# Kernel optimization log

Hardware: AMD Instinct MI355X
Metric: run time of the kernel (lower is better)

The kernel has to match this reference:

```python
import jax, jax.numpy as jnp
import numpy as np

HEADS = 64
VOCAB = 5
EPS = 1e-5

def _layer_norm(x, g, b):
    mu = jnp.mean(x, axis=-1, keepdims=True)
    var = jnp.var(x, axis=-1, keepdims=True)
    return (x - mu) * jax.lax.rsqrt(var + EPS) * g + b

def setup_inputs() -> dict:
    key = jax.random.key(0)
    ks = jax.random.split(key, 12)
    h = HEADS
    s = 1.0 / np.sqrt(h)
    return {
        "x": jax.random.normal(ks[0], (8, 384, 384, h), dtype=jnp.float32),
        "W1": jax.random.normal(ks[1], (h, h), dtype=jnp.float32) * s,
        "b1": jnp.zeros((h,), jnp.float32),
        "W2": jax.random.normal(ks[2], (h, h), dtype=jnp.float32) * s,
        "b2": jnp.zeros((h,), jnp.float32),
        "W3": jax.random.normal(ks[3], (h, h), dtype=jnp.float32) * s,
        "b3": jnp.zeros((h,), jnp.float32),
        "ln_g": jnp.ones((h,), jnp.float32),
        "ln_b": jnp.zeros((h,), jnp.float32),
        "Wo": jax.random.normal(ks[4], (h, VOCAB), dtype=jnp.float32) * s,
        "bo": jnp.zeros((VOCAB,), jnp.float32),
    }

def reference(x, W1, b1, W2, b2, W3, b3, ln_g, ln_b, Wo, bo):
    # three (Linear -> gelu -> shared LayerNorm) blocks on [b,s,s,h]
    h = _layer_norm(jax.nn.gelu(x @ W1 + b1, approximate=False), ln_g, ln_b)
    h = _layer_norm(jax.nn.gelu(h @ W2 + b2, approximate=False), ln_g, ln_b)
    h = _layer_norm(jax.nn.gelu(h @ W3 + b3, approximate=False), ln_g, ln_b)
    out = h @ Wo + bo  # [b,s,s,vocab]
    return (out + jnp.swapaxes(out, 1, 2)) * 0.5
```

## Files before the change

kernel.cpp:

```cpp
#include <hip/hip_runtime.h>
#include <cstdint>
#include <cstddef>

typedef __attribute__((ext_vector_type(8))) __bf16   bf16x8;
typedef __attribute__((ext_vector_type(2))) __bf16   bf16x2;
typedef __attribute__((ext_vector_type(4))) float    f32x4;
typedef __attribute__((ext_vector_type(4))) uint32_t u32x4;

#define N_ROWS   1179648
#define N_TILES  73728
#define BLOCKS   2048
#define TPW      9
#define SDIM     384
#define VOCAB    5

#define WO_OFF   24576
#define BIAS_OFF 26624
#define OUT_OFF  27392

__device__ __forceinline__ f32x4 gelu4(f32x4 x){
  f32x4 u = x * x;
  f32x4 w = u * (-0.10294456f) + (-2.3021255f);
  f32x4 z = x * w;
  f32x4 e;
  e[0] = __builtin_amdgcn_exp2f(z[0]);
  e[1] = __builtin_amdgcn_exp2f(z[1]);
  e[2] = __builtin_amdgcn_exp2f(z[2]);
  e[3] = __builtin_amdgcn_exp2f(z[3]);
  f32x4 d = e + 1.0f;
  f32x4 r;
  r[0] = __builtin_amdgcn_rcpf(d[0]);
  r[1] = __builtin_amdgcn_rcpf(d[1]);
  r[2] = __builtin_amdgcn_rcpf(d[2]);
  r[3] = __builtin_amdgcn_rcpf(d[3]);
  return x * r;
}

__device__ __forceinline__ bf16x8 mk_bf8(f32x4 a, f32x4 b){
  bf16x8 v;
  v[0]=(__bf16)a[0]; v[1]=(__bf16)a[1]; v[2]=(__bf16)a[2]; v[3]=(__bf16)a[3];
  v[4]=(__bf16)b[0]; v[5]=(__bf16)b[1]; v[6]=(__bf16)b[2]; v[7]=(__bf16)b[3];
  return v;
}

__device__ __forceinline__ int perm_rho(int m){
  return (m & 0x23) | ((m & 4) << 2) | ((m & 0x18) >> 1);
}

__global__ __launch_bounds__(256)
void mlp_kernel(const float* __restrict__ x,
                const float* __restrict__ W1, const float* __restrict__ b1,
                const float* __restrict__ W2, const float* __restrict__ b2,
                const float* __restrict__ W3, const float* __restrict__ b3,
                const float* __restrict__ lng, const float* __restrict__ lnb,
                const float* __restrict__ Wo,  const float* __restrict__ bo,
                float* __restrict__ tmp)
{
  __shared__ __align__(16) uint8_t Wl[28672];

  const int tid = threadIdx.x;

  {
    int m = tid & 63, g = tid >> 6;
    int rho = perm_rho(m);
    uint8_t* wrow = Wl + rho * 128;
    int swz = (rho & 7) << 4;
    #pragma unroll 1
    for (int idx = g; idx < 96; idx += 4) {
      int L = idx >> 5, kp = idx & 31;
      const float* W = (L == 0) ? W1 : ((L == 1) ? W2 : W3);
      float lo = W[(2 * kp    ) * 64 + m];
      float hi = W[(2 * kp + 1) * 64 + m];
      bf16x2 p = { (__bf16)lo, (__bf16)hi };
      *(uint32_t*)(wrow + L * 8192 + ((4 * kp) ^ swz)) = __builtin_bit_cast(uint32_t, p);
    }
    int mm = tid & 15;
    #pragma unroll 1
    for (int kp = tid >> 4; kp < 32; kp += 16) {
      float lo = (mm < VOCAB) ? Wo[(2 * kp    ) * VOCAB + mm] : 0.0f;
      float hi = (mm < VOCAB) ? Wo[(2 * kp + 1) * VOCAB + mm] : 0.0f;
      bf16x2 p = { (__bf16)lo, (__bf16)hi };
      *(uint32_t*)(Wl + WO_OFF + mm * 128 + ((4 * kp) ^ ((mm & 7) << 4))) =
          __builtin_bit_cast(uint32_t, p);
    }
    if (tid < 192) {
      float v = (tid < 64) ? b1[tid] : ((tid < 128) ? b2[tid - 64] : b3[tid - 128]);
      *(float*)(Wl + BIAS_OFF + tid * 4) = v;
    }
  }
  __syncthreads();

  const int wav  = tid >> 6, lane = tid & 63;
  const int h    = lane >> 4;
  const int b    = lane & 15;
  const int swzW = (b & 7) << 4;
  const int rowB = b * 128;
  const int kOff = 16 * h;
  const float* biasL = (const float*)(Wl + BIAS_OFF);
  float* myF = (float*)(Wl + OUT_OFF) + wav * 80;

  f32x4 ggr[4], bbr[4], aoInit;
  #pragma unroll
  for (int mt = 0; mt < 4; ++mt) {
    int base = 8 * h + 4 * (mt & 1) + 32 * (mt >> 1);
    ggr[mt] = *(const f32x4*)(lng + base);
    bbr[mt] = *(const f32x4*)(lnb + base);
  }
  #pragma unroll
  for (int r = 0; r < 4; ++r) {
    int v = 4 * h + r;
    aoInit[r] = (v < VOCAB) ? bo[v] : 0.0f;
  }

  const int gw = blockIdx.x * 4 + wav;
  int t = gw * TPW;

  f32x4 xn[4];
  {
    const float* px = x + (size_t)(t * 16 + b) * 64 + 8 * h;
    xn[0] = *(const f32x4*)(px);      xn[1] = *(const f32x4*)(px + 4);
    xn[2] = *(const f32x4*)(px + 32); xn[3] = *(const f32x4*)(px + 36);
  }

  #pragma unroll 1
  for (int i = 0; i < TPW; ++i, ++t) {
    u32x4 bfr[2];
    bfr[0] = __builtin_bit_cast(u32x4, mk_bf8(xn[0], xn[1]));
    bfr[1] = __builtin_bit_cast(u32x4, mk_bf8(xn[2], xn[3]));

    {
      int tn = (i + 1 < TPW) ? (t + 1) : t;
      const float* pn = x + (size_t)(tn * 16 + b) * 64 + 8 * h;
      xn[0] = *(const f32x4*)(pn);      xn[1] = *(const f32x4*)(pn + 4);
      xn[2] = *(const f32x4*)(pn + 32); xn[3] = *(const f32x4*)(pn + 36);
    }

    #pragma unroll
    for (int L = 0; L < 3; ++L) {
      const uint8_t* wp = Wl + L * 8192 + rowB;
      f32x4 acc[4];
      #pragma unroll
      for (int mt = 0; mt < 4; ++mt) {
        u32x4 w0 = *(const u32x4*)(wp + mt * 2048 + ((kOff     ) ^ swzW));
        u32x4 w1 = *(const u32x4*)(wp + mt * 2048 + ((kOff + 64) ^ swzW));
        int base = 8 * h + 4 * (mt & 1) + 32 * (mt >> 1);
        acc[mt] = *(const f32x4*)(biasL + L * 64 + base);
        acc[mt] = __builtin_amdgcn_mfma_f32_16x16x32_bf16(
            __builtin_bit_cast(bf16x8, w0), __builtin_bit_cast(bf16x8, bfr[0]), acc[mt], 0, 0, 0);
        acc[mt] = __builtin_amdgcn_mfma_f32_16x16x32_bf16(
            __builtin_bit_cast(bf16x8, w1), __builtin_bit_cast(bf16x8, bfr[1]), acc[mt], 0, 0, 0);
      }

      #pragma unroll
      for (int mt = 0; mt < 4; ++mt) acc[mt] = gelu4(acc[mt]);

      f32x4 vs = acc[0] + acc[1] + acc[2] + acc[3];
      f32x4 vq = acc[0]*acc[0] + acc[1]*acc[1] + acc[2]*acc[2] + acc[3]*acc[3];
      float s1 = (vs[0]+vs[1]) + (vs[2]+vs[3]);
      float s2 = (vq[0]+vq[1]) + (vq[2]+vq[3]);
      s1 += __shfl_xor(s1, 16); s2 += __shfl_xor(s2, 16);
      s1 += __shfl_xor(s1, 32); s2 += __shfl_xor(s2, 32);
      float mu   = s1 * (1.0f/64.0f);
      float var  = __builtin_fmaf(s2, (1.0f/64.0f), -mu * mu);
      float rstd = rsqrtf(var + 1e-5f);
      float nm   = -mu * rstd;

      f32x4 n0 = (acc[0] * rstd + nm) * ggr[0] + bbr[0];
      f32x4 n1 = (acc[1] * rstd + nm) * ggr[1] + bbr[1];
      f32x4 n2 = (acc[2] * rstd + nm) * ggr[2] + bbr[2];
      f32x4 n3 = (acc[3] * rstd + nm) * ggr[3] + bbr[3];
      bfr[0] = __builtin_bit_cast(u32x4, mk_bf8(n0, n1));
      bfr[1] = __builtin_bit_cast(u32x4, mk_bf8(n2, n3));
    }

    f32x4 ao = aoInit;
    {
      const uint8_t* wp = Wl + WO_OFF + rowB;
      u32x4 w0 = *(const u32x4*)(wp + ((kOff     ) ^ swzW));
      u32x4 w1 = *(const u32x4*)(wp + ((kOff + 64) ^ swzW));
      ao = __builtin_amdgcn_mfma_f32_16x16x32_bf16(
          __builtin_bit_cast(bf16x8, w0), __builtin_bit_cast(bf16x8, bfr[0]), ao, 0, 0, 0);
      ao = __builtin_amdgcn_mfma_f32_16x16x32_bf16(
          __builtin_bit_cast(bf16x8, w1), __builtin_bit_cast(bf16x8, bfr[1]), ao, 0, 0, 0);
    }

    #pragma unroll
    for (int r = 0; r < 4; ++r) {
      int v = 4 * h + r;
      if (v < VOCAB) myF[b * VOCAB + v] = ao[r];
    }
    float* dst = tmp + (size_t)t * 80;
    dst[lane] = myF[lane];
    if (lane < 16) dst[64 + lane] = myF[64 + lane];
  }
}

__global__ __launch_bounds__(256)
void sym_kernel(const float* __restrict__ tmp, float* __restrict__ out)
{
  __shared__ float A[32][164];
  __shared__ float B[32][164];
  int bid = blockIdx.x;
  int bb = bid / 144, r2 = bid - bb * 144;
  int ti = r2 / 12,  tj = r2 - ti * 12;
  int i0 = ti * 32,  j0 = tj * 32;
  const size_t base = (size_t)bb * SDIM * SDIM;

  for (int idx = threadIdx.x; idx < 32 * 160; idx += 256) {
    int r = idx / 160, c = idx - r * 160;
    A[r][c] = tmp[(base + (size_t)(i0 + r) * SDIM + j0) * VOCAB + c];
    B[r][c] = tmp[(base + (size_t)(j0 + r) * SDIM + i0) * VOCAB + c];
  }
  __syncthreads();
  for (int idx = threadIdx.x; idx < 32 * 160; idx += 256) {
    int r = idx / 160, c = idx - r * 160;
    int jc = c / 5, v = c - jc * 5;
    out[(base + (size_t)(i0 + r) * SDIM + j0) * VOCAB + c] =
        0.5f * (A[r][c] + B[jc][r * 5 + v]);
  }
}

extern "C" void kernel_launch(void* const* d_in, const int* in_sizes, int n_in,
                              void* d_out, int out_size, void* d_ws, size_t ws_size,
                              hipStream_t stream)
{
  const float* x   = (const float*)d_in[0];
  const float* W1  = (const float*)d_in[1];
  const float* b1  = (const float*)d_in[2];
  const float* W2  = (const float*)d_in[3];
  const float* b2  = (const float*)d_in[4];
  const float* W3  = (const float*)d_in[5];
  const float* b3  = (const float*)d_in[6];
  const float* lng = (const float*)d_in[7];
  const float* lnb = (const float*)d_in[8];
  const float* Wo  = (const float*)d_in[9];
  const float* bo  = (const float*)d_in[10];

  float* tmp = (float*)d_ws;
  float* out = (float*)d_out;

  mlp_kernel<<<BLOCKS, 256, 0, stream>>>(x, W1, b1, W2, b2, W3, b3,
                                         lng, lnb, Wo, bo, tmp);
  sym_kernel<<<8 * 12 * 12, 256, 0, stream>>>(tmp, out);
}
```

Before: 147.7 us.

## Fuse symmetrization into MLP kernel using paired transposed 16x16 tiles per block

Merges the MLP and symmetrization kernels into one. Each block computes a 16x16 (i,j) tile together with its transposed (j,i) partner, or two diagonal tiles, keeps the logits in LDS and writes the symmetrized output directly. This drops the workspace round trip and the second launch. In exchange, LDS use grows, each wave now reads rows spread across the grid instead of contiguous ones, and the block count changes from 2048 to 2304.

```diff
diff --git a/kernel.cpp b/kernel.cpp
--- a/kernel.cpp
+++ b/kernel.cpp
@@ -7,12 +7,11 @@
 typedef __attribute__((ext_vector_type(4))) float    f32x4;
 typedef __attribute__((ext_vector_type(4))) uint32_t u32x4;
 
-#define N_ROWS   1179648
-#define N_TILES  73728
-#define BLOCKS   2048
-#define TPW      9
 #define SDIM     384
 #define VOCAB    5
+#define SPW      8
+#define WGPB     288
+#define BLOCKS   (8 * WGPB)
 
 #define WO_OFF   24576
 #define BIAS_OFF 26624
@@ -48,15 +47,15 @@
 }
 
 __global__ __launch_bounds__(256)
-void mlp_kernel(const float* __restrict__ x,
-                const float* __restrict__ W1, const float* __restrict__ b1,
-                const float* __restrict__ W2, const float* __restrict__ b2,
-                const float* __restrict__ W3, const float* __restrict__ b3,
-                const float* __restrict__ lng, const float* __restrict__ lnb,
-                const float* __restrict__ Wo,  const float* __restrict__ bo,
-                float* __restrict__ tmp)
+void mlp_sym_kernel(const float* __restrict__ x,
+                    const float* __restrict__ W1, const float* __restrict__ b1,
+                    const float* __restrict__ W2, const float* __restrict__ b2,
+                    const float* __restrict__ W3, const float* __restrict__ b3,
+                    const float* __restrict__ lng, const float* __restrict__ lnb,
+                    const float* __restrict__ Wo,  const float* __restrict__ bo,
+                    float* __restrict__ out)
 {
-  __shared__ __align__(16) uint8_t Wl[28672];
+  __shared__ __align__(16) uint8_t Wl[37632];
 
   const int tid = threadIdx.x;
 
@@ -90,6 +89,20 @@
   }
   __syncthreads();
 
+  const int bb  = blockIdx.x / WGPB;
+  const int rem = blockIdx.x - bb * WGPB;
+  int I0, J0, I1, J1;
+  bool diag;
+  if (rem < 276) {
+    int I = 0, acc = 0;
+    while (acc + (23 - I) <= rem) { acc += 23 - I; ++I; }
+    int J = I + 1 + (rem - acc);
+    I0 = I << 4; J0 = J << 4; I1 = J << 4; J1 = I << 4; diag = false;
+  } else {
+    int d = rem - 276;
+    I0 = J0 = (2 * d) << 4; I1 = J1 = (2 * d + 1) << 4; diag = true;
+  }
+
   const int wav  = tid >> 6, lane = tid & 63;
   const int h    = lane >> 4;
   const int b    = lane & 15;
@@ -97,7 +110,12 @@
   const int rowB = b * 128;
   const int kOff = 16 * h;
   const float* biasL = (const float*)(Wl + BIAS_OFF);
-  float* myF = (float*)(Wl + OUT_OFF) + wav * 80;
+  float* outS = (float*)(Wl + OUT_OFF);
+
+  const int blk  = wav >> 1, half = wav & 1;
+  const int rowb = (blk ? I1 : I0) + 8 * half;
+  const int colb = (blk ? J1 : J0);
+  const long base0 = ((long)(bb * SDIM + rowb)) * SDIM + colb;
 
   f32x4 ggr[4], bbr[4], aoInit;
   #pragma unroll
@@ -112,25 +130,22 @@
     aoInit[r] = (v < VOCAB) ? bo[v] : 0.0f;
   }
 
-  const int gw = blockIdx.x * 4 + wav;
-  int t = gw * TPW;
-
   f32x4 xn[4];
   {
-    const float* px = x + (size_t)(t * 16 + b) * 64 + 8 * h;
+    const float* px = x + (size_t)(base0 + b) * 64 + 8 * h;
     xn[0] = *(const f32x4*)(px);      xn[1] = *(const f32x4*)(px + 4);
     xn[2] = *(const f32x4*)(px + 32); xn[3] = *(const f32x4*)(px + 36);
   }
 
   #pragma unroll 1
-  for (int i = 0; i < TPW; ++i, ++t) {
+  for (int i = 0; i < SPW; ++i) {
     u32x4 bfr[2];
     bfr[0] = __builtin_bit_cast(u32x4, mk_bf8(xn[0], xn[1]));
     bfr[1] = __builtin_bit_cast(u32x4, mk_bf8(xn[2], xn[3]));
 
     {
-      int tn = (i + 1 < TPW) ? (t + 1) : t;
-      const float* pn = x + (size_t)(tn * 16 + b) * 64 + 8 * h;
+      int inext = (i + 1 < SPW) ? (i + 1) : i;
+      const float* pn = x + (size_t)(base0 + inext * SDIM + b) * 64 + 8 * h;
       xn[0] = *(const f32x4*)(pn);      xn[1] = *(const f32x4*)(pn + 4);
       xn[2] = *(const f32x4*)(pn + 32); xn[3] = *(const f32x4*)(pn + 36);
     }
@@ -184,39 +199,29 @@
           __builtin_bit_cast(bf16x8, w1), __builtin_bit_cast(bf16x8, bfr[1]), ao, 0, 0, 0);
     }
 
+    float* myF = outS + blk * 1280 + (8 * half + i) * 80;
     #pragma unroll
     for (int r = 0; r < 4; ++r) {
       int v = 4 * h + r;
       if (v < VOCAB) myF[b * VOCAB + v] = ao[r];
     }
-    float* dst = tmp + (size_t)t * 80;
-    dst[lane] = myF[lane];
-    if (lane < 16) dst[64 + lane] = myF[64 + lane];
-  }
-}
-
-__global__ __launch_bounds__(256)
-void sym_kernel(const float* __restrict__ tmp, float* __restrict__ out)
-{
-  __shared__ float A[32][164];
-  __shared__ float B[32][164];
-  int bid = blockIdx.x;
-  int bb = bid / 144, r2 = bid - bb * 144;
-  int ti = r2 / 12,  tj = r2 - ti * 12;
-  int i0 = ti * 32,  j0 = tj * 32;
-  const size_t base = (size_t)bb * SDIM * SDIM;
-
-  for (int idx = threadIdx.x; idx < 32 * 160; idx += 256) {
-    int r = idx / 160, c = idx - r * 160;
-    A[r][c] = tmp[(base + (size_t)(i0 + r) * SDIM + j0) * VOCAB + c];
-    B[r][c] = tmp[(base + (size_t)(j0 + r) * SDIM + i0) * VOCAB + c];
   }
   __syncthreads();
-  for (int idx = threadIdx.x; idx < 32 * 160; idx += 256) {
-    int r = idx / 160, c = idx - r * 160;
-    int jc = c / 5, v = c - jc * 5;
-    out[(base + (size_t)(i0 + r) * SDIM + j0) * VOCAB + c] =
-        0.5f * (A[r][c] + B[jc][r * 5 + v]);
+
+  #pragma unroll 1
+  for (int idx = tid; idx < 2560; idx += 256) {
+    int bk = (idx >= 1280) ? 1 : 0;
+    int q2 = idx - bk * 1280;
+    int r  = q2 / 80;
+    int q  = q2 - r * 80;
+    int c  = q / 5;
+    int v  = q - c * 5;
+    int pb = diag ? bk : 1 - bk;
+    float val = 0.5f * (outS[bk * 1280 + r * 80 + q] +
+                        outS[pb * 1280 + c * 80 + r * 5 + v]);
+    int ii = (bk ? I1 : I0) + r;
+    int jj = (bk ? J1 : J0) + c;
+    out[((size_t)(bb * SDIM + ii) * SDIM + jj) * VOCAB + v] = val;
   }
 }
 
@@ -236,10 +241,8 @@
   const float* Wo  = (const float*)d_in[9];
   const float* bo  = (const float*)d_in[10];
 
-  float* tmp = (float*)d_ws;
   float* out = (float*)d_out;
 
-  mlp_kernel<<<BLOCKS, 256, 0, stream>>>(x, W1, b1, W2, b2, W3, b3,
-                                         lng, lnb, Wo, bo, tmp);
-  sym_kernel<<<8 * 12 * 12, 256, 0, stream>>>(tmp, out);
-}
+  mlp_sym_kernel<<<BLOCKS, 256, 0, stream>>>(x, W1, b1, W2, b2, W3, b3,
+                                             lng, lnb, Wo, bo, out);
+}
```

Result: faster. 136.8 us, median of 2 (-7.4%).
